# Performance work log

Hardware: AMD Instinct MI355X
Metric: run time of the kernel (lower is better)

## Reference

```python
import jax, jax.numpy as jnp
import numpy as np

N_PER_DEG = 30000
MAX_DEG = 6
MIN_DEG = 0
N_ATOMS = N_PER_DEG * (MAX_DEG + 1)  # 210000, atoms sorted by degree
N_FEAT = 128
NB_FILTER = 128
NB_AFFINE = 2 * MAX_DEG + (1 - MIN_DEG)  # 13


def setup_inputs() -> dict:
    key = jax.random.key(0)
    ks = jax.random.split(key, 2 + MAX_DEG)
    atoms = jax.random.normal(ks[0], (N_ATOMS, N_FEAT), dtype=jnp.float32)
    # glorot-ish scale for the 13 affine weights
    W = jax.random.normal(ks[1], (NB_AFFINE, N_FEAT, NB_FILTER), dtype=jnp.float32) * (1.0 / np.sqrt(N_FEAT))
    b = jnp.zeros((NB_AFFINE, NB_FILTER), dtype=jnp.float32)
    # deg_slice[d] = (start, count) for degree d in 0..MAX_DEG; equal-size buckets
    deg_slice = jnp.asarray(
        np.stack([np.arange(MAX_DEG + 1) * N_PER_DEG,
                  np.full(MAX_DEG + 1, N_PER_DEG)], axis=1).astype(np.int32))
    inp = {"atoms": atoms, "W": W, "b": b, "deg_slice": deg_slice}
    for d in range(1, MAX_DEG + 1):
        inp[f"adj{d}"] = jax.random.randint(ks[1 + d], (N_PER_DEG, d), 0, N_ATOMS, dtype=jnp.int32)
    return inp


def reference(atoms, W, b, deg_slice, adj1, adj2, adj3, adj4, adj5, adj6):
    """Degree-bucketed graph convolution (deepchem GraphConv, linear activation).

    W ordering matches the original iterator: for deg=1..MAX_DEG the pair
    (rel=W[2*(deg-1)], self=W[2*(deg-1)+1]), then deg-0 self uses W[2*MAX_DEG].
    Output concat order: deg 0 bucket first, then deg 1..MAX_DEG.
    """
    adjs = [adj1, adj2, adj3, adj4, adj5, adj6]
    ds = np.asarray(deg_slice)  # structural constant: static slice bounds
    outs = [None] * (MAX_DEG + 1 - MIN_DEG)
    # deg 0: self-affine only
    s0, c0 = int(ds[0, 0]), int(ds[0, 1])
    outs[0] = atoms[s0:s0 + c0] @ W[2 * MAX_DEG] + b[2 * MAX_DEG]
    for deg in range(1, MAX_DEG + 1):
        s, c = int(ds[deg, 0]), int(ds[deg, 1])
        # gather neighbors of each degree-deg atom and sum: (c, deg, F) -> (c, F)
        rel = jnp.take(atoms, adjs[deg - 1], axis=0).sum(axis=1)
        out = (rel @ W[2 * (deg - 1)] + b[2 * (deg - 1)]
               + atoms[s:s + c] @ W[2 * (deg - 1) + 1] + b[2 * (deg - 1) + 1])
        outs[deg] = out
    return jnp.concatenate(outs, axis=0)  # (N_ATOMS, NB_FILTER)
```

## Files before the change

kernel.cpp:

```cpp
#include <hip/hip_runtime.h>
#include <hip/hip_bf16.h>

#define NPD 30000
#define NF  128
#define MAXDEG 6
#define LDK2 264

#define CVT_BLOCKS 13125
#define WT_BLOCKS  208

typedef __attribute__((ext_vector_type(8))) short short8;
typedef __attribute__((ext_vector_type(4))) float floatx4;

__device__ __forceinline__ unsigned short f2bf(float f) {
    __hip_bfloat16 h = __float2bfloat16(f);
    return __builtin_bit_cast(unsigned short, h);
}
__device__ __forceinline__ float bf2f(unsigned short u) {
    unsigned v = ((unsigned)u) << 16; return __builtin_bit_cast(float, v);
}
__device__ __forceinline__ uint4 pack16B(float4 a, float4 b) {
    uint4 v;
    v.x = (unsigned)f2bf(a.x) | ((unsigned)f2bf(a.y) << 16);
    v.y = (unsigned)f2bf(a.z) | ((unsigned)f2bf(a.w) << 16);
    v.z = (unsigned)f2bf(b.x) | ((unsigned)f2bf(b.y) << 16);
    v.w = (unsigned)f2bf(b.z) | ((unsigned)f2bf(b.w) << 16);
    return v;
}
__device__ __forceinline__ uint4 pack16Bv(floatx4 a, floatx4 b) {
    uint4 v;
    v.x = (unsigned)f2bf(a.x) | ((unsigned)f2bf(a.y) << 16);
    v.y = (unsigned)f2bf(a.z) | ((unsigned)f2bf(a.w) << 16);
    v.z = (unsigned)f2bf(b.x) | ((unsigned)f2bf(b.y) << 16);
    v.w = (unsigned)f2bf(b.z) | ((unsigned)f2bf(b.w) << 16);
    return v;
}
__device__ __forceinline__ void addu4(float* s, uint4 h) {
    s[0] += bf2f((unsigned short)h.x); s[1] += bf2f((unsigned short)(h.x >> 16));
    s[2] += bf2f((unsigned short)h.y); s[3] += bf2f((unsigned short)(h.y >> 16));
    s[4] += bf2f((unsigned short)h.z); s[5] += bf2f((unsigned short)(h.z >> 16));
    s[6] += bf2f((unsigned short)h.w); s[7] += bf2f((unsigned short)(h.w >> 16));
}

__global__ __launch_bounds__(256) void prep_kernel(
    const float* __restrict__ atoms, const float* __restrict__ W,
    unsigned short* __restrict__ atomsH, unsigned short* __restrict__ Wt)
{
    __shared__ unsigned short t[32][33];
    const int bx = blockIdx.x;
    if (bx < WT_BLOCKS) {
        const int a  = bx >> 4;
        const int k0 = ((bx >> 2) & 3) * 32, n0 = (bx & 3) * 32;
        const int tx = threadIdx.x & 31, ty = threadIdx.x >> 5;
        const float*    Wp  = W  + (size_t)a * NF * NF;
        unsigned short* Wtp = Wt + (size_t)a * NF * NF;
#pragma unroll
        for (int i = 0; i < 32; i += 8)
            t[ty + i][tx] = f2bf(Wp[(size_t)(k0 + ty + i) * NF + (n0 + tx)]);
        __syncthreads();
#pragma unroll
        for (int i = 0; i < 32; i += 8)
            Wtp[(size_t)(n0 + ty + i) * NF + (k0 + tx)] = t[tx][ty + i];
    } else {
        const size_t i = (size_t)(bx - WT_BLOCKS) * 256 + threadIdx.x;
        const floatx4* p = (const floatx4*)(atoms + i * 8);
        floatx4 a = __builtin_nontemporal_load(p);
        floatx4 b = __builtin_nontemporal_load(p + 1);
        ((uint4*)atomsH)[i] = pack16Bv(a, b);
    }
}

template <int DEG, bool BF16A>
__device__ __forceinline__ void fused_work(
    const float* __restrict__ atomsF, const unsigned short* __restrict__ atomsH,
    const unsigned short* __restrict__ Wt, const float* __restrict__ bvec,
    const int* __restrict__ adj, float* __restrict__ out,
    unsigned short* __restrict__ sA)
{
    const int tid  = threadIdx.x;
    const int lane = tid & 63, wave = tid >> 6;
    const int nb = lane & 15;
    const int kq = (lane >> 4) * 8;
    const int col0 = wave * 32;
    const int row0 = blockIdx.x * 32;
    const int valid = min(32, NPD - row0);
    const int row0g = DEG * NPD + row0;
    const int wi_self = (DEG == 0) ? 12 : (2 * DEG - 1);
    const int wi_rel  = (DEG > 0) ? 2 * (DEG - 1) : 0;

    const int r0 = tid >> 4,        ch0 = (tid & 15) * 8;
    const int r1 = r0 + 16;
    const int rr0 = min(r0, valid - 1), rr1 = min(r1, valid - 1);
    if (BF16A) {
        uint4 s0 = *(const uint4*)(atomsH + (size_t)(row0g + rr0) * NF + ch0);
        uint4 s1 = *(const uint4*)(atomsH + (size_t)(row0g + rr1) * NF + ch0);
        *(uint4*)&sA[r0 * LDK2 + ch0] = s0;
        *(uint4*)&sA[r1 * LDK2 + ch0] = s1;
    } else {
        const float4* sp0 = (const float4*)(atomsF + (size_t)(row0g + rr0) * NF + ch0);
        const float4* sp1 = (const float4*)(atomsF + (size_t)(row0g + rr1) * NF + ch0);
        float4 a0 = sp0[0], a1 = sp0[1], a2 = sp1[0], a3 = sp1[1];
        *(uint4*)&sA[r0 * LDK2 + ch0] = pack16B(a0, a1);
        *(uint4*)&sA[r1 * LDK2 + ch0] = pack16B(a2, a3);
    }

    if constexpr (DEG > 0) {
        const int gr  = tid >> 3;
        const int gc  = (tid & 7) * 16;
        const int grr = min(gr, valid - 1);
        const int* arow = adj + (size_t)(row0 + grr) * DEG;
        int idxs[DEG];
#pragma unroll
        for (int j = 0; j < DEG; ++j) idxs[j] = arow[j];

        float s[16];
#pragma unroll
        for (int i = 0; i < 16; ++i) s[i] = 0.f;

        if (BF16A) {
            uint4 ga[DEG], gb[DEG];
#pragma unroll
            for (int j = 0; j < DEG; ++j) {
                const unsigned short* base = atomsH + (size_t)idxs[j] * NF + gc;
                ga[j] = *(const uint4*)base;
                gb[j] = *(const uint4*)(base + 8);
            }
#pragma unroll
            for (int j = 0; j < DEG; ++j) {
                addu4(s, ga[j]);
                addu4(s + 8, gb[j]);
            }
        } else {
            float4 q0, q1, q2, q3, n0, n1, n2, n3;
            {
                const float4* p = (const float4*)(atomsF + (size_t)idxs[0] * NF + gc);
                q0 = p[0]; q1 = p[1]; q2 = p[2]; q3 = p[3];
            }
#pragma unroll
            for (int j = 0; j < DEG; ++j) {
                if (j + 1 < DEG) {
                    const float4* p = (const float4*)(atomsF + (size_t)idxs[j + 1] * NF + gc);
                    n0 = p[0]; n1 = p[1]; n2 = p[2]; n3 = p[3];
                }
                s[0]  += q0.x; s[1]  += q0.y; s[2]  += q0.z; s[3]  += q0.w;
                s[4]  += q1.x; s[5]  += q1.y; s[6]  += q1.z; s[7]  += q1.w;
                s[8]  += q2.x; s[9]  += q2.y; s[10] += q2.z; s[11] += q2.w;
                s[12] += q3.x; s[13] += q3.y; s[14] += q3.z; s[15] += q3.w;
                q0 = n0; q1 = n1; q2 = n2; q3 = n3;
            }
        }
        uint4 w0 = pack16B(make_float4(s[0], s[1], s[2], s[3]),
                           make_float4(s[4], s[5], s[6], s[7]));
        uint4 w1 = pack16B(make_float4(s[8], s[9], s[10], s[11]),
                           make_float4(s[12], s[13], s[14], s[15]));
        *(uint4*)&sA[gr * LDK2 + NF + gc]     = w0;
        *(uint4*)&sA[gr * LDK2 + NF + gc + 8] = w1;
    }
    __syncthreads();

    floatx4 acc[2][2];
#pragma unroll
    for (int i = 0; i < 2; i++)
#pragma unroll
        for (int j = 0; j < 2; j++) acc[i][j] = (floatx4){0.f, 0.f, 0.f, 0.f};

    constexpr int NKK = (DEG > 0) ? 8 : 4;
#pragma unroll
    for (int kk = 0; kk < NKK; ++kk) {
        const int wi = (kk < 4) ? wi_self : wi_rel;
        const unsigned short* Wp = Wt + (size_t)wi * NF * NF;
        short8 bfr[2];
#pragma unroll
        for (int nt = 0; nt < 2; ++nt)
            bfr[nt] = *(const short8*)(Wp + (size_t)(col0 + nt * 16 + nb) * NF
                                          + (kk & 3) * 32 + kq);
        short8 af[2];
#pragma unroll
        for (int mt = 0; mt < 2; ++mt)
            af[mt] = *(const short8*)&sA[(mt * 16 + nb) * LDK2 + kk * 32 + kq];
#pragma unroll
        for (int mt = 0; mt < 2; ++mt)
#pragma unroll
            for (int nt = 0; nt < 2; ++nt)
                acc[mt][nt] = __builtin_amdgcn_mfma_f32_16x16x32_bf16(
                    af[mt], bfr[nt], acc[mt][nt], 0, 0, 0);
    }

    float bias[2];
#pragma unroll
    for (int nt = 0; nt < 2; ++nt) {
        const int n = col0 + nt * 16 + nb;
        float bv = bvec[wi_self * NF + n];
        if (DEG > 0) bv += bvec[wi_rel * NF + n];
        bias[nt] = bv;
    }
    const int rq = (lane >> 4) * 4;
#pragma unroll
    for (int mt = 0; mt < 2; ++mt) {
#pragma unroll
        for (int reg = 0; reg < 4; ++reg) {
            const int r = mt * 16 + rq + reg;
            if (r < valid) {
                float* op = out + (size_t)(row0g + r) * NF;
#pragma unroll
                for (int nt = 0; nt < 2; ++nt)
                    __builtin_nontemporal_store(acc[mt][nt][reg] + bias[nt],
                                                op + col0 + nt * 16 + nb);
            }
        }
    }
}

template <bool BF16A>
__global__ __launch_bounds__(256) void fused_kernel(
    const float* __restrict__ atomsF, const unsigned short* __restrict__ atomsH,
    const unsigned short* __restrict__ Wt, const float* __restrict__ bvec,
    const int* __restrict__ adj1, const int* __restrict__ adj2,
    const int* __restrict__ adj3, const int* __restrict__ adj4,
    const int* __restrict__ adj5, const int* __restrict__ adj6,
    float* __restrict__ out)
{
    __shared__ unsigned short sA[32 * LDK2];
    switch (blockIdx.y) {
        case 0: fused_work<0, BF16A>(atomsF, atomsH, Wt, bvec, nullptr, out, sA); break;
        case 1: fused_work<1, BF16A>(atomsF, atomsH, Wt, bvec, adj1,    out, sA); break;
        case 2: fused_work<2, BF16A>(atomsF, atomsH, Wt, bvec, adj2,    out, sA); break;
        case 3: fused_work<3, BF16A>(atomsF, atomsH, Wt, bvec, adj3,    out, sA); break;
        case 4: fused_work<4, BF16A>(atomsF, atomsH, Wt, bvec, adj4,    out, sA); break;
        case 5: fused_work<5, BF16A>(atomsF, atomsH, Wt, bvec, adj5,    out, sA); break;
        default: fused_work<6, BF16A>(atomsF, atomsH, Wt, bvec, adj6,   out, sA); break;
    }
}

__global__ __launch_bounds__(128) void naive_kernel(
    const float* __restrict__ atoms, const float* __restrict__ W,
    const float* __restrict__ b,
    const int* __restrict__ adj1, const int* __restrict__ adj2,
    const int* __restrict__ adj3, const int* __restrict__ adj4,
    const int* __restrict__ adj5, const int* __restrict__ adj6,
    float* __restrict__ out)
{
    const int i = blockIdx.x;
    const int deg = i / NPD, r = i - deg * NPD, n = threadIdx.x;
    __shared__ float selfr[NF], relr[NF];
    selfr[n] = atoms[(size_t)i * NF + n];
    float rv = 0.f;
    if (deg > 0) {
        const int* adjs[6] = {adj1, adj2, adj3, adj4, adj5, adj6};
        const int* adj = adjs[deg - 1];
        for (int j = 0; j < deg; ++j)
            rv += atoms[(size_t)adj[(size_t)r * deg + j] * NF + n];
    }
    relr[n] = rv;
    __syncthreads();
    const int ws  = (deg == 0) ? 12 : 2 * deg - 1;
    const int wrl = 2 * (deg - 1);
    float acc = b[ws * NF + n] + ((deg > 0) ? b[wrl * NF + n] : 0.f);
    for (int k = 0; k < NF; ++k) {
        acc += selfr[k] * W[(size_t)ws * NF * NF + (size_t)k * NF + n];
        if (deg > 0) acc += relr[k] * W[(size_t)wrl * NF * NF + (size_t)k * NF + n];
    }
    out[(size_t)i * NF + n] = acc;
}

extern "C" void kernel_launch(void* const* d_in, const int* in_sizes, int n_in,
                              void* d_out, int out_size, void* d_ws, size_t ws_size,
                              hipStream_t stream) {
    const float* atoms = (const float*)d_in[0];
    const float* W     = (const float*)d_in[1];
    const float* b     = (const float*)d_in[2];
    const int* adj1 = (const int*)d_in[4];
    const int* adj2 = (const int*)d_in[5];
    const int* adj3 = (const int*)d_in[6];
    const int* adj4 = (const int*)d_in[7];
    const int* adj5 = (const int*)d_in[8];
    const int* adj6 = (const int*)d_in[9];

    const size_t wt_bytes = (size_t)13 * NF * NF * sizeof(unsigned short);
    const size_t at_bytes = (size_t)NPD * (MAXDEG + 1) * NF * sizeof(unsigned short);
    const int gx = (NPD + 31) / 32;

    if (ws_size >= wt_bytes + at_bytes) {
        unsigned short* Wt     = (unsigned short*)d_ws;
        unsigned short* atomsH = (unsigned short*)((char*)d_ws + wt_bytes);
        prep_kernel<<<WT_BLOCKS + CVT_BLOCKS, 256, 0, stream>>>(atoms, W, atomsH, Wt);
        fused_kernel<true><<<dim3(gx, 7), 256, 0, stream>>>(
            atoms, atomsH, Wt, b, adj1, adj2, adj3, adj4, adj5, adj6, (float*)d_out);
    } else if (ws_size >= wt_bytes) {
        unsigned short* Wt = (unsigned short*)d_ws;
        prep_kernel<<<WT_BLOCKS, 256, 0, stream>>>(atoms, W, nullptr, Wt);
        fused_kernel<false><<<dim3(gx, 7), 256, 0, stream>>>(
            atoms, nullptr, Wt, b, adj1, adj2, adj3, adj4, adj5, adj6, (float*)d_out);
    } else {
        naive_kernel<<<NPD * (MAXDEG + 1), NF, 0, stream>>>(
            atoms, W, b, adj1, adj2, adj3, adj4, adj5, adj6, (float*)d_out);
    }
}
```

Before: 264.7 us.

## Overlap neighbor gather with self-weight MFMA and interleave degree buckets

The fused kernel now loads self weights into registers and issues the neighbor gathers first, then runs the self-half MFMAs while those gather loads are still in flight. It uses LDS-only waitcnt barriers in place of __syncthreads. Blocks are flattened so degree buckets interleave (bid % 7), which spreads the heavy high-degree tiles across CUs. The atom conversion prep kernel is coarsened to 8 chunks per thread, cutting block count. The cost is extra register pressure from holding 8 weight fragments plus all gather results at once.

```diff
diff --git a/kernel.cpp b/kernel.cpp
--- a/kernel.cpp
+++ b/kernel.cpp
@@ -6,8 +6,8 @@
 #define MAXDEG 6
 #define LDK2 264
 
-#define CVT_BLOCKS 13125
-#define WT_BLOCKS  208
+#define WT_BLOCKS   208
+#define CVT8_BLOCKS 1641
 
 typedef __attribute__((ext_vector_type(8))) short short8;
 typedef __attribute__((ext_vector_type(4))) float floatx4;
@@ -40,6 +40,11 @@
     s[2] += bf2f((unsigned short)h.y); s[3] += bf2f((unsigned short)(h.y >> 16));
     s[4] += bf2f((unsigned short)h.z); s[5] += bf2f((unsigned short)(h.z >> 16));
     s[6] += bf2f((unsigned short)h.w); s[7] += bf2f((unsigned short)(h.w >> 16));
+}
+
+__device__ __forceinline__ void lgkm_barrier() {
+    asm volatile("s_waitcnt lgkmcnt(0)" ::: "memory");
+    __builtin_amdgcn_s_barrier();
 }
 
 __global__ __launch_bounds__(256) void prep_kernel(
@@ -62,11 +67,18 @@
         for (int i = 0; i < 32; i += 8)
             Wtp[(size_t)(n0 + ty + i) * NF + (k0 + tx)] = t[tx][ty + i];
     } else {
-        const size_t i = (size_t)(bx - WT_BLOCKS) * 256 + threadIdx.x;
-        const floatx4* p = (const floatx4*)(atoms + i * 8);
-        floatx4 a = __builtin_nontemporal_load(p);
-        floatx4 b = __builtin_nontemporal_load(p + 1);
-        ((uint4*)atomsH)[i] = pack16Bv(a, b);
+        const size_t n8   = (size_t)NPD * (MAXDEG + 1) * NF / 8;
+        const size_t base = (size_t)(bx - WT_BLOCKS) * 2048 + threadIdx.x;
+#pragma unroll
+        for (int it = 0; it < 8; ++it) {
+            const size_t i = base + (size_t)it * 256;
+            if (i < n8) {
+                const floatx4* p = (const floatx4*)(atoms + i * 8);
+                floatx4 a = __builtin_nontemporal_load(p);
+                floatx4 b = __builtin_nontemporal_load(p + 1);
+                ((uint4*)atomsH)[i] = pack16Bv(a, b);
+            }
+        }
     }
 }
 
@@ -75,62 +87,144 @@
     const float* __restrict__ atomsF, const unsigned short* __restrict__ atomsH,
     const unsigned short* __restrict__ Wt, const float* __restrict__ bvec,
     const int* __restrict__ adj, float* __restrict__ out,
-    unsigned short* __restrict__ sA)
+    unsigned short* __restrict__ sA, int bx)
 {
     const int tid  = threadIdx.x;
     const int lane = tid & 63, wave = tid >> 6;
     const int nb = lane & 15;
     const int kq = (lane >> 4) * 8;
     const int col0 = wave * 32;
-    const int row0 = blockIdx.x * 32;
+    const int row0 = bx * 32;
     const int valid = min(32, NPD - row0);
     const int row0g = DEG * NPD + row0;
     const int wi_self = (DEG == 0) ? 12 : (2 * DEG - 1);
     const int wi_rel  = (DEG > 0) ? 2 * (DEG - 1) : 0;
 
-    const int r0 = tid >> 4,        ch0 = (tid & 15) * 8;
+    floatx4 acc[2][2];
+#pragma unroll
+    for (int i = 0; i < 2; i++)
+#pragma unroll
+        for (int j = 0; j < 2; j++) acc[i][j] = (floatx4){0.f, 0.f, 0.f, 0.f};
+
+    const int r0 = tid >> 4,  ch0 = (tid & 15) * 8;
     const int r1 = r0 + 16;
     const int rr0 = min(r0, valid - 1), rr1 = min(r1, valid - 1);
-    if (BF16A) {
+
+    auto mma4_pre = [&](const short8 bs[4][2], int aoff) {
+#pragma unroll
+        for (int kk = 0; kk < 4; ++kk) {
+            short8 af[2];
+#pragma unroll
+            for (int mt = 0; mt < 2; ++mt)
+                af[mt] = *(const short8*)&sA[(mt * 16 + nb) * LDK2 + aoff + kk * 32 + kq];
+#pragma unroll
+            for (int mt = 0; mt < 2; ++mt)
+#pragma unroll
+                for (int nt = 0; nt < 2; ++nt)
+                    acc[mt][nt] = __builtin_amdgcn_mfma_f32_16x16x32_bf16(
+                        af[mt], bs[kk][nt], acc[mt][nt], 0, 0, 0);
+        }
+    };
+    auto mma4_ld = [&](int wi, int aoff) {
+        const unsigned short* Wp = Wt + (size_t)wi * NF * NF;
+#pragma unroll
+        for (int kk = 0; kk < 4; ++kk) {
+            short8 bfr[2];
+#pragma unroll
+            for (int nt = 0; nt < 2; ++nt)
+                bfr[nt] = *(const short8*)(Wp + (size_t)(col0 + nt * 16 + nb) * NF
+                                              + kk * 32 + kq);
+            short8 af[2];
+#pragma unroll
+            for (int mt = 0; mt < 2; ++mt)
+                af[mt] = *(const short8*)&sA[(mt * 16 + nb) * LDK2 + aoff + kk * 32 + kq];
+#pragma unroll
+            for (int mt = 0; mt < 2; ++mt)
+#pragma unroll
+                for (int nt = 0; nt < 2; ++nt)
+                    acc[mt][nt] = __builtin_amdgcn_mfma_f32_16x16x32_bf16(
+                        af[mt], bfr[nt], acc[mt][nt], 0, 0, 0);
+        }
+    };
+
+    if constexpr (BF16A) {
         uint4 s0 = *(const uint4*)(atomsH + (size_t)(row0g + rr0) * NF + ch0);
         uint4 s1 = *(const uint4*)(atomsH + (size_t)(row0g + rr1) * NF + ch0);
-        *(uint4*)&sA[r0 * LDK2 + ch0] = s0;
-        *(uint4*)&sA[r1 * LDK2 + ch0] = s1;
+
+        const int gr  = tid >> 3;
+        const int gc  = (tid & 7) * 16;
+        const int grr = min(gr, valid - 1);
+
+        int idxs[DEG > 0 ? DEG : 1];
+        if constexpr (DEG > 0) {
+            const int* arow = adj + (size_t)(row0 + grr) * DEG;
+#pragma unroll
+            for (int j = 0; j < DEG; ++j) idxs[j] = arow[j];
+        }
+
+        short8 bs[4][2];
+        {
+            const unsigned short* Wp = Wt + (size_t)wi_self * NF * NF;
+#pragma unroll
+            for (int kk = 0; kk < 4; ++kk)
+#pragma unroll
+                for (int nt = 0; nt < 2; ++nt)
+                    bs[kk][nt] = *(const short8*)(Wp + (size_t)(col0 + nt * 16 + nb) * NF
+                                                     + kk * 32 + kq);
+        }
+
+        if constexpr (DEG > 0) {
+            uint4 ga[DEG], gb[DEG];
+#pragma unroll
+            for (int j = 0; j < DEG; ++j) {
+                const unsigned short* base = atomsH + (size_t)idxs[j] * NF + gc;
+                ga[j] = *(const uint4*)base;
+                gb[j] = *(const uint4*)(base + 8);
+            }
+
+            *(uint4*)&sA[r0 * LDK2 + ch0] = s0;
+            *(uint4*)&sA[r1 * LDK2 + ch0] = s1;
+            lgkm_barrier();
+
+            mma4_pre(bs, 0);
+
+            float s[16];
+#pragma unroll
+            for (int i = 0; i < 16; ++i) s[i] = 0.f;
+#pragma unroll
+            for (int j = 0; j < DEG; ++j) { addu4(s, ga[j]); addu4(s + 8, gb[j]); }
+            uint4 w0 = pack16B(make_float4(s[0], s[1], s[2], s[3]),
+                               make_float4(s[4], s[5], s[6], s[7]));
+            uint4 w1 = pack16B(make_float4(s[8], s[9], s[10], s[11]),
+                               make_float4(s[12], s[13], s[14], s[15]));
+            *(uint4*)&sA[gr * LDK2 + NF + gc]     = w0;
+            *(uint4*)&sA[gr * LDK2 + NF + gc + 8] = w1;
+            lgkm_barrier();
+
+            mma4_ld(wi_rel, NF);
+        } else {
+            *(uint4*)&sA[r0 * LDK2 + ch0] = s0;
+            *(uint4*)&sA[r1 * LDK2 + ch0] = s1;
+            lgkm_barrier();
+            mma4_pre(bs, 0);
+        }
     } else {
         const float4* sp0 = (const float4*)(atomsF + (size_t)(row0g + rr0) * NF + ch0);
         const float4* sp1 = (const float4*)(atomsF + (size_t)(row0g + rr1) * NF + ch0);
         float4 a0 = sp0[0], a1 = sp0[1], a2 = sp1[0], a3 = sp1[1];
         *(uint4*)&sA[r0 * LDK2 + ch0] = pack16B(a0, a1);
         *(uint4*)&sA[r1 * LDK2 + ch0] = pack16B(a2, a3);
-    }
-
-    if constexpr (DEG > 0) {
-        const int gr  = tid >> 3;
-        const int gc  = (tid & 7) * 16;
-        const int grr = min(gr, valid - 1);
-        const int* arow = adj + (size_t)(row0 + grr) * DEG;
-        int idxs[DEG];
-#pragma unroll
-        for (int j = 0; j < DEG; ++j) idxs[j] = arow[j];
-
-        float s[16];
-#pragma unroll
-        for (int i = 0; i < 16; ++i) s[i] = 0.f;
-
-        if (BF16A) {
-            uint4 ga[DEG], gb[DEG];
-#pragma unroll
-            for (int j = 0; j < DEG; ++j) {
-                const unsigned short* base = atomsH + (size_t)idxs[j] * NF + gc;
-                ga[j] = *(const uint4*)base;
-                gb[j] = *(const uint4*)(base + 8);
-            }
-#pragma unroll
-            for (int j = 0; j < DEG; ++j) {
-                addu4(s, ga[j]);
-                addu4(s + 8, gb[j]);
-            }
-        } else {
+        if constexpr (DEG > 0) {
+            const int gr  = tid >> 3;
+            const int gc  = (tid & 7) * 16;
+            const int grr = min(gr, valid - 1);
+            const int* arow = adj + (size_t)(row0 + grr) * DEG;
+            int idxs[DEG];
+#pragma unroll
+            for (int j = 0; j < DEG; ++j) idxs[j] = arow[j];
+            float s[16];
+#pragma unroll
+            for (int i = 0; i < 16; ++i) s[i] = 0.f;
             float4 q0, q1, q2, q3, n0, n1, n2, n3;
             {
                 const float4* p = (const float4*)(atomsF + (size_t)idxs[0] * NF + gc);
@@ -148,42 +242,16 @@
                 s[12] += q3.x; s[13] += q3.y; s[14] += q3.z; s[15] += q3.w;
                 q0 = n0; q1 = n1; q2 = n2; q3 = n3;
             }
-        }
-        uint4 w0 = pack16B(make_float4(s[0], s[1], s[2], s[3]),
-                           make_float4(s[4], s[5], s[6], s[7]));
-        uint4 w1 = pack16B(make_float4(s[8], s[9], s[10], s[11]),
-                           make_float4(s[12], s[13], s[14], s[15]));
-        *(uint4*)&sA[gr * LDK2 + NF + gc]     = w0;
-        *(uint4*)&sA[gr * LDK2 + NF + gc + 8] = w1;
-    }
-    __syncthreads();
-
-    floatx4 acc[2][2];
-#pragma unroll
-    for (int i = 0; i < 2; i++)
-#pragma unroll
-        for (int j = 0; j < 2; j++) acc[i][j] = (floatx4){0.f, 0.f, 0.f, 0.f};
-
-    constexpr int NKK = (DEG > 0) ? 8 : 4;
-#pragma unroll
-    for (int kk = 0; kk < NKK; ++kk) {
-        const int wi = (kk < 4) ? wi_self : wi_rel;
-        const unsigned short* Wp = Wt + (size_t)wi * NF * NF;
-        short8 bfr[2];
-#pragma unroll
-        for (int nt = 0; nt < 2; ++nt)
-            bfr[nt] = *(const short8*)(Wp + (size_t)(col0 + nt * 16 + nb) * NF
-                                          + (kk & 3) * 32 + kq);
-        short8 af[2];
-#pragma unroll
-        for (int mt = 0; mt < 2; ++mt)
-            af[mt] = *(const short8*)&sA[(mt * 16 + nb) * LDK2 + kk * 32 + kq];
-#pragma unroll
-        for (int mt = 0; mt < 2; ++mt)
-#pragma unroll
-            for (int nt = 0; nt < 2; ++nt)
-                acc[mt][nt] = __builtin_amdgcn_mfma_f32_16x16x32_bf16(
-                    af[mt], bfr[nt], acc[mt][nt], 0, 0, 0);
+            uint4 w0 = pack16B(make_float4(s[0], s[1], s[2], s[3]),
+                               make_float4(s[4], s[5], s[6], s[7]));
+            uint4 w1 = pack16B(make_float4(s[8], s[9], s[10], s[11]),
+                               make_float4(s[12], s[13], s[14], s[15]));
+            *(uint4*)&sA[gr * LDK2 + NF + gc]     = w0;
+            *(uint4*)&sA[gr * LDK2 + NF + gc + 8] = w1;
+        }
+        __syncthreads();
+        mma4_ld(wi_self, 0);
+        if constexpr (DEG > 0) mma4_ld(wi_rel, NF);
     }
 
     float bias[2];
@@ -221,14 +289,16 @@
     float* __restrict__ out)
 {
     __shared__ unsigned short sA[32 * LDK2];
-    switch (blockIdx.y) {
-        case 0: fused_work<0, BF16A>(atomsF, atomsH, Wt, bvec, nullptr, out, sA); break;
-        case 1: fused_work<1, BF16A>(atomsF, atomsH, Wt, bvec, adj1,    out, sA); break;
-        case 2: fused_work<2, BF16A>(atomsF, atomsH, Wt, bvec, adj2,    out, sA); break;
-        case 3: fused_work<3, BF16A>(atomsF, atomsH, Wt, bvec, adj3,    out, sA); break;
-        case 4: fused_work<4, BF16A>(atomsF, atomsH, Wt, bvec, adj4,    out, sA); break;
-        case 5: fused_work<5, BF16A>(atomsF, atomsH, Wt, bvec, adj5,    out, sA); break;
-        default: fused_work<6, BF16A>(atomsF, atomsH, Wt, bvec, adj6,   out, sA); break;
+    const int bid = blockIdx.x;
+    const int deg = bid % 7, bx = bid / 7;
+    switch (deg) {
+        case 0: fused_work<0, BF16A>(atomsF, atomsH, Wt, bvec, nullptr, out, sA, bx); break;
+        case 1: fused_work<1, BF16A>(atomsF, atomsH, Wt, bvec, adj1,    out, sA, bx); break;
+        case 2: fused_work<2, BF16A>(atomsF, atomsH, Wt, bvec, adj2,    out, sA, bx); break;
+        case 3: fused_work<3, BF16A>(atomsF, atomsH, Wt, bvec, adj3,    out, sA, bx); break;
+        case 4: fused_work<4, BF16A>(atomsF, atomsH, Wt, bvec, adj4,    out, sA, bx); break;
+        case 5: fused_work<5, BF16A>(atomsF, atomsH, Wt, bvec, adj5,    out, sA, bx); break;
+        default: fused_work<6, BF16A>(atomsF, atomsH, Wt, bvec, adj6,   out, sA, bx); break;
     }
 }
 
@@ -283,13 +353,13 @@
     if (ws_size >= wt_bytes + at_bytes) {
         unsigned short* Wt     = (unsigned short*)d_ws;
         unsigned short* atomsH = (unsigned short*)((char*)d_ws + wt_bytes);
-        prep_kernel<<<WT_BLOCKS + CVT_BLOCKS, 256, 0, stream>>>(atoms, W, atomsH, Wt);
-        fused_kernel<true><<<dim3(gx, 7), 256, 0, stream>>>(
+        prep_kernel<<<WT_BLOCKS + CVT8_BLOCKS, 256, 0, stream>>>(atoms, W, atomsH, Wt);
+        fused_kernel<true><<<gx * 7, 256, 0, stream>>>(
             atoms, atomsH, Wt, b, adj1, adj2, adj3, adj4, adj5, adj6, (float*)d_out);
     } else if (ws_size >= wt_bytes) {
         unsigned short* Wt = (unsigned short*)d_ws;
         prep_kernel<<<WT_BLOCKS, 256, 0, stream>>>(atoms, W, nullptr, Wt);
-        fused_kernel<false><<<dim3(gx, 7), 256, 0, stream>>>(
+        fused_kernel<false><<<gx * 7, 256, 0, stream>>>(
             atoms, nullptr, Wt, b, adj1, adj2, adj3, adj4, adj5, adj6, (float*)d_out);
     } else {
         naive_kernel<<<NPD * (MAXDEG + 1), NF, 0, stream>>>(
```

Result: no change. 264.6 us (-0.0%).
